# Performance work log

Hardware: AMD Instinct MI355X
Metric: run time of the kernel (lower is better)

## Reference

```python
import jax, jax.numpy as jnp
import numpy as np

B, S, D = 4, 2048, 2048
E = 64           # num_experts
TOPK = 2         # num_experts_per_token


def setup_inputs() -> dict:
    key = jax.random.key(0)
    k1, k2, k3 = jax.random.split(key, 3)
    x_real = jax.random.normal(k1, (B, S, D), dtype=jnp.float32)
    x_imag = jax.random.normal(k2, (B, S, D), dtype=jnp.float32)
    # flax Dense: kernel [in_features, out_features] with lecun_normal-ish scale
    W = jax.random.normal(k3, (2 * D, E), dtype=jnp.float32) / np.sqrt(2.0 * D)
    b = jnp.zeros((E,), dtype=jnp.float32)
    return {"x_real": x_real, "x_imag": x_imag, "W": W, "b": b}


def reference(x_real, x_imag, W, b):
    # amp = |x|, phase = angle(x) for x = x_real + i*x_imag
    amp = jnp.hypot(x_real, x_imag)                 # [B,S,D]
    phase = jnp.arctan2(x_imag, x_real)             # [B,S,D]
    routing_input = jnp.concatenate([amp, phase], axis=-1)  # [B,S,2D]
    scores = jnp.einsum('bsf,fe->bse', routing_input, W) + b  # [B,S,E]
    probs = jax.nn.softmax(scores, axis=-1)
    top_k_probs, top_k_indices = jax.lax.top_k(probs, TOPK)   # [B,S,K]
    top_k_probs = top_k_probs / jnp.sum(top_k_probs, axis=-1, keepdims=True)
    return (top_k_probs, top_k_indices)
```

## Files before the change

kernel.cpp:

```cpp
#include <hip/hip_runtime.h>
#include <math.h>

#define NTOK 8192
#define DD   2048
#define EE   64
#define TSTRIP 16
#define PROB_N (NTOK*2)
#define F_PSTRIDE (128*4*64*8)

typedef _Float16 f16x8 __attribute__((ext_vector_type(8)));
typedef _Float16 f16x4 __attribute__((ext_vector_type(4)));
typedef float    f32x4 __attribute__((ext_vector_type(4)));

__device__ __forceinline__ float fast_atan2f(float y, float x) {
    const float ax = __builtin_fabsf(x), ay = __builtin_fabsf(y);
    const float hi = fmaxf(ax, ay), lo = fminf(ax, ay);
    const bool  big = lo > 0.4142135679721832f * hi;
    const float num = big ? (lo - hi) : lo;
    const float den = big ? (lo + hi) : hi;
    float rc = __builtin_amdgcn_rcpf(den);
    rc = rc * fmaf(-den, rc, 2.0f);
    const float z  = num * rc;
    const float z2 = z * z;
    float p = fmaf(z2, 8.05374449538e-2f, -1.38776856032e-1f);
    p = fmaf(z2, p, 1.99777106478e-1f);
    p = fmaf(z2, p, -3.33329491539e-1f);
    float r = fmaf(z * z2, p, z);
    r = r + (big ? 0.78539816339744830962f : 0.0f);
    r = (ay > ax) ? (1.57079632679489661923f - r) : r;
    r = (x < 0.0f) ? (3.14159265358979323846f - r) : r;
    return copysignf(r, y);
}

__device__ __forceinline__ void fsplit2(float x, _Float16& h1, _Float16& h2s) {
    const _Float16 a = (_Float16)x;
    h1 = a;
    h2s = (_Float16)((x - (float)a) * 2048.0f);
}

__global__ __launch_bounds__(256) void wsplit(const float* __restrict__ W,
                                              _Float16* __restrict__ F) {
    const int g  = blockIdx.x * 256 + threadIdx.x;
    const int e  = g & 63;
    const int q  = g >> 6;
    const int d0 = q * 4;
    const int nt = e >> 4;
    const int lane = ((d0 & 31) >> 3) * 16 + (e & 15);
    const int j0 = d0 & 7;
    const int cka = 2 * (d0 >> 5);

    f16x4 a1, a2, p1, p2;
    #pragma unroll
    for (int i = 0; i < 4; ++i) {
        _Float16 h, l;
        fsplit2(W[(size_t)(d0 + i) * EE + e], h, l);      a1[i] = h; a2[i] = l;
        fsplit2(W[(size_t)(DD + d0 + i) * EE + e], h, l); p1[i] = h; p2[i] = l;
    }
    *(f16x4*)&F[((size_t)(0 * 128 + cka)     * 4 + nt) * 512 + lane * 8 + j0] = a1;
    *(f16x4*)&F[((size_t)(1 * 128 + cka)     * 4 + nt) * 512 + lane * 8 + j0] = a2;
    *(f16x4*)&F[((size_t)(0 * 128 + cka + 1) * 4 + nt) * 512 + lane * 8 + j0] = p1;
    *(f16x4*)&F[((size_t)(1 * 128 + cka + 1) * 4 + nt) * 512 + lane * 8 + j0] = p2;
}

__global__ __launch_bounds__(512) void gemm_topk(
    const float* __restrict__ xr, const float* __restrict__ xi,
    const _Float16* __restrict__ F, const float* __restrict__ bias,
    float* __restrict__ out)
{
    __shared__ float scoreP[8][TSTRIP][EE];

    const int tid = threadIdx.x;
    const int t0  = blockIdx.x * TSTRIP;
    const int wv = tid >> 6, lane = tid & 63;
    const int fm = lane & 15, fq = lane >> 4;

    const float* prx = xr + (size_t)(t0 + fm) * DD + wv * 256 + fq * 8;
    const float* pix = xi + (size_t)(t0 + fm) * DD + wv * 256 + fq * 8;

    f32x4 accH[4], accL[4];
    #pragma unroll
    for (int nt = 0; nt < 4; ++nt) {
        accH[nt] = (f32x4){0.f, 0.f, 0.f, 0.f};
        accL[nt] = (f32x4){0.f, 0.f, 0.f, 0.f};
    }

    #pragma unroll 2
    for (int p = 0; p < 8; ++p) {
        const float4 r0 = *(const float4*)(prx + p * 32);
        const float4 r1 = *(const float4*)(prx + p * 32 + 4);
        const float4 i0 = *(const float4*)(pix + p * 32);
        const float4 i1 = *(const float4*)(pix + p * 32 + 4);

        f16x8 a1, a2, q1, q2;
        #pragma unroll
        for (int h = 0; h < 2; ++h) {
            const float4 vr = h ? r1 : r0;
            const float4 vi = h ? i1 : i0;
            const float ar[4] = {vr.x, vr.y, vr.z, vr.w};
            const float ai[4] = {vi.x, vi.y, vi.z, vi.w};
            #pragma unroll
            for (int i = 0; i < 4; ++i) {
                const float amp = __builtin_amdgcn_sqrtf(fmaf(ar[i], ar[i], ai[i] * ai[i]));
                const float ph  = fast_atan2f(ai[i], ar[i]);
                _Float16 hh, ll;
                fsplit2(amp, hh, ll); a1[h * 4 + i] = hh; a2[h * 4 + i] = ll;
                fsplit2(ph,  hh, ll); q1[h * 4 + i] = hh; q2[h * 4 + i] = ll;
            }
        }

        const int ck = (wv * 8 + p) * 2;
        const _Float16* bp = F + ((size_t)ck * 4) * 512 + lane * 8;
        #pragma unroll
        for (int nt = 0; nt < 4; ++nt) {
            const _Float16* qp = bp + nt * 512;
            const f16x8 b1a = *(const f16x8*)(qp);
            const f16x8 b2a = *(const f16x8*)(qp + F_PSTRIDE);
            const f16x8 b1p = *(const f16x8*)(qp + 2048);
            const f16x8 b2p = *(const f16x8*)(qp + 2048 + F_PSTRIDE);
            accH[nt] = __builtin_amdgcn_mfma_f32_16x16x32_f16(a1, b1a, accH[nt], 0, 0, 0);
            accL[nt] = __builtin_amdgcn_mfma_f32_16x16x32_f16(a1, b2a, accL[nt], 0, 0, 0);
            accL[nt] = __builtin_amdgcn_mfma_f32_16x16x32_f16(a2, b1a, accL[nt], 0, 0, 0);
            accH[nt] = __builtin_amdgcn_mfma_f32_16x16x32_f16(q1, b1p, accH[nt], 0, 0, 0);
            accL[nt] = __builtin_amdgcn_mfma_f32_16x16x32_f16(q1, b2p, accL[nt], 0, 0, 0);
            accL[nt] = __builtin_amdgcn_mfma_f32_16x16x32_f16(q2, b1p, accL[nt], 0, 0, 0);
        }
    }

    #pragma unroll
    for (int nt = 0; nt < 4; ++nt)
        #pragma unroll
        for (int r = 0; r < 4; ++r)
            scoreP[wv][fq * 4 + r][nt * 16 + fm] =
                fmaf(accL[nt][r], 4.8828125e-4f, accH[nt][r]);
    __syncthreads();

    const float bv = bias[lane];
    #pragma unroll
    for (int rep = 0; rep < 2; ++rep) {
        const int tok = wv * 2 + rep;
        float v1 = bv;
        #pragma unroll
        for (int kq = 0; kq < 8; ++kq) v1 += scoreP[kq][tok][lane];
        float v2 = -INFINITY;
        int   i1 = lane, i2 = 64;
        #pragma unroll
        for (int off = 1; off < 64; off <<= 1) {
            const float ov1 = __shfl_xor(v1, off, 64);
            const int   oi1 = __shfl_xor(i1, off, 64);
            const float ov2 = __shfl_xor(v2, off, 64);
            const int   oi2 = __shfl_xor(i2, off, 64);
            const bool b1 = (ov1 > v1) || (ov1 == v1 && oi1 < i1);
            const float n1 = b1 ? ov1 : v1;  const int ni1 = b1 ? oi1 : i1;
            const float c1 = b1 ? v1  : ov1; const int ci1 = b1 ? i1  : oi1;
            const float c2 = b1 ? ov2 : v2;  const int ci2 = b1 ? oi2 : i2;
            const bool b2 = (c1 > c2) || (c1 == c2 && ci1 < ci2);
            v1 = n1; i1 = ni1;
            v2 = b2 ? c1 : c2; i2 = b2 ? ci1 : ci2;
        }
        if (lane == 0) {
            const int t = t0 + tok;
            const float z  = expf(v2 - v1);
            const float p1 = 1.0f / (1.0f + z);
            const float p2 = z / (1.0f + z);
            out[(size_t)t * 2 + 0] = p1;
            out[(size_t)t * 2 + 1] = p2;
            out[PROB_N + (size_t)t * 2 + 0] = (float)i1;
            out[PROB_N + (size_t)t * 2 + 1] = (float)i2;
        }
    }
}

extern "C" void kernel_launch(void* const* d_in, const int* in_sizes, int n_in,
                              void* d_out, int out_size, void* d_ws, size_t ws_size,
                              hipStream_t stream) {
    const float* xr = (const float*)d_in[0];
    const float* xi = (const float*)d_in[1];
    const float* W  = (const float*)d_in[2];
    const float* b  = (const float*)d_in[3];
    float* out = (float*)d_out;
    _Float16* F = (_Float16*)d_ws;

    wsplit<<<128, 256, 0, stream>>>(W, F);
    gemm_topk<<<NTOK / TSTRIP, 512, 0, stream>>>(xr, xi, F, b, out);
}
```

Measured before the change: 175.2 us.

## Software-pipeline x and weight loads with inline-asm global loads and vmcnt waits

```diff
diff --git a/kernel.cpp b/kernel.cpp
--- a/kernel.cpp
+++ b/kernel.cpp
@@ -11,6 +11,21 @@
 typedef _Float16 f16x8 __attribute__((ext_vector_type(8)));
 typedef _Float16 f16x4 __attribute__((ext_vector_type(4)));
 typedef float    f32x4 __attribute__((ext_vector_type(4)));
+
+__device__ __forceinline__ f16x8 gload_f16x8(const _Float16* p) {
+    f16x8 r;
+    asm volatile("global_load_dwordx4 %0, %1, off" : "=v"(r) : "v"(p));
+    return r;
+}
+__device__ __forceinline__ f32x4 gload_f32x4(const float* p) {
+    f32x4 r;
+    asm volatile("global_load_dwordx4 %0, %1, off" : "=v"(r) : "v"(p));
+    return r;
+}
+#define VMWAIT(n) do { \
+    asm volatile("s_waitcnt vmcnt(" #n ")" ::: "memory"); \
+    __builtin_amdgcn_sched_barrier(0); \
+} while (0)
 
 __device__ __forceinline__ float fast_atan2f(float y, float x) {
     const float ax = __builtin_fabsf(x), ay = __builtin_fabsf(y);
@@ -76,6 +91,7 @@
 
     const float* prx = xr + (size_t)(t0 + fm) * DD + wv * 256 + fq * 8;
     const float* pix = xi + (size_t)(t0 + fm) * DD + wv * 256 + fq * 8;
+    const _Float16* bp0 = F + (size_t)wv * 32768 + lane * 8;
 
     f32x4 accH[4], accL[4];
     #pragma unroll
@@ -84,39 +100,71 @@
         accL[nt] = (f32x4){0.f, 0.f, 0.f, 0.f};
     }
 
-    #pragma unroll 2
+    f32x4 xv[2][4];
+    f16x8 bb[2][16];
+
+    xv[0][0] = gload_f32x4(prx);
+    xv[0][1] = gload_f32x4(prx + 4);
+    xv[0][2] = gload_f32x4(pix);
+    xv[0][3] = gload_f32x4(pix + 4);
+    #pragma unroll
+    for (int nt = 0; nt < 4; ++nt) {
+        bb[0][nt * 4 + 0] = gload_f16x8(bp0 + nt * 512);
+        bb[0][nt * 4 + 1] = gload_f16x8(bp0 + nt * 512 + F_PSTRIDE);
+        bb[0][nt * 4 + 2] = gload_f16x8(bp0 + nt * 512 + 2048);
+        bb[0][nt * 4 + 3] = gload_f16x8(bp0 + nt * 512 + 2048 + F_PSTRIDE);
+    }
+    xv[1][0] = gload_f32x4(prx + 32);
+    xv[1][1] = gload_f32x4(prx + 36);
+    xv[1][2] = gload_f32x4(pix + 32);
+    xv[1][3] = gload_f32x4(pix + 36);
+
+    #pragma unroll 8
     for (int p = 0; p < 8; ++p) {
-        const float4 r0 = *(const float4*)(prx + p * 32);
-        const float4 r1 = *(const float4*)(prx + p * 32 + 4);
-        const float4 i0 = *(const float4*)(pix + p * 32);
-        const float4 i1 = *(const float4*)(pix + p * 32 + 4);
+        const int s = p & 1, ns = s ^ 1;
+
+        if (p < 7) { VMWAIT(20); } else { VMWAIT(16); }
 
         f16x8 a1, a2, q1, q2;
-        #pragma unroll
-        for (int h = 0; h < 2; ++h) {
-            const float4 vr = h ? r1 : r0;
-            const float4 vi = h ? i1 : i0;
-            const float ar[4] = {vr.x, vr.y, vr.z, vr.w};
-            const float ai[4] = {vi.x, vi.y, vi.z, vi.w};
+        {
+            const f32x4 vr0 = xv[s][0], vr1 = xv[s][1];
+            const f32x4 vi0 = xv[s][2], vi1 = xv[s][3];
             #pragma unroll
             for (int i = 0; i < 4; ++i) {
-                const float amp = __builtin_amdgcn_sqrtf(fmaf(ar[i], ar[i], ai[i] * ai[i]));
-                const float ph  = fast_atan2f(ai[i], ar[i]);
+                float rr = vr0[i], im = vi0[i];
+                float amp = __builtin_amdgcn_sqrtf(fmaf(rr, rr, im * im));
+                float ph  = fast_atan2f(im, rr);
                 _Float16 hh, ll;
-                fsplit2(amp, hh, ll); a1[h * 4 + i] = hh; a2[h * 4 + i] = ll;
-                fsplit2(ph,  hh, ll); q1[h * 4 + i] = hh; q2[h * 4 + i] = ll;
+                fsplit2(amp, hh, ll); a1[i] = hh; a2[i] = ll;
+                fsplit2(ph,  hh, ll); q1[i] = hh; q2[i] = ll;
+                rr = vr1[i]; im = vi1[i];
+                amp = __builtin_amdgcn_sqrtf(fmaf(rr, rr, im * im));
+                ph  = fast_atan2f(im, rr);
+                fsplit2(amp, hh, ll); a1[4 + i] = hh; a2[4 + i] = ll;
+                fsplit2(ph,  hh, ll); q1[4 + i] = hh; q2[4 + i] = ll;
             }
         }
 
-        const int ck = (wv * 8 + p) * 2;
-        const _Float16* bp = F + ((size_t)ck * 4) * 512 + lane * 8;
+        if (p < 7) {
+            const _Float16* nb = bp0 + (size_t)(p + 1) * 4096;
+            #pragma unroll
+            for (int nt = 0; nt < 4; ++nt) {
+                bb[ns][nt * 4 + 0] = gload_f16x8(nb + nt * 512);
+                bb[ns][nt * 4 + 1] = gload_f16x8(nb + nt * 512 + F_PSTRIDE);
+                bb[ns][nt * 4 + 2] = gload_f16x8(nb + nt * 512 + 2048);
+                bb[ns][nt * 4 + 3] = gload_f16x8(nb + nt * 512 + 2048 + F_PSTRIDE);
+            }
+            VMWAIT(20);
+        } else {
+            VMWAIT(0);
+        }
+
         #pragma unroll
         for (int nt = 0; nt < 4; ++nt) {
-            const _Float16* qp = bp + nt * 512;
-            const f16x8 b1a = *(const f16x8*)(qp);
-            const f16x8 b2a = *(const f16x8*)(qp + F_PSTRIDE);
-            const f16x8 b1p = *(const f16x8*)(qp + 2048);
-            const f16x8 b2p = *(const f16x8*)(qp + 2048 + F_PSTRIDE);
+            const f16x8 b1a = bb[s][nt * 4 + 0];
+            const f16x8 b2a = bb[s][nt * 4 + 1];
+            const f16x8 b1p = bb[s][nt * 4 + 2];
+            const f16x8 b2p = bb[s][nt * 4 + 3];
             accH[nt] = __builtin_amdgcn_mfma_f32_16x16x32_f16(a1, b1a, accH[nt], 0, 0, 0);
             accL[nt] = __builtin_amdgcn_mfma_f32_16x16x32_f16(a1, b2a, accL[nt], 0, 0, 0);
             accL[nt] = __builtin_amdgcn_mfma_f32_16x16x32_f16(a2, b1a, accL[nt], 0, 0, 0);
@@ -124,6 +172,13 @@
             accL[nt] = __builtin_amdgcn_mfma_f32_16x16x32_f16(q1, b2p, accL[nt], 0, 0, 0);
             accL[nt] = __builtin_amdgcn_mfma_f32_16x16x32_f16(q2, b1p, accL[nt], 0, 0, 0);
         }
+
+        if (p < 6) {
+            xv[s][0] = gload_f32x4(prx + (p + 2) * 32);
+            xv[s][1] = gload_f32x4(prx + (p + 2) * 32 + 4);
+            xv[s][2] = gload_f32x4(pix + (p + 2) * 32);
+            xv[s][3] = gload_f32x4(pix + (p + 2) * 32 + 4);
+        }
     }
 
     #pragma unroll
@@ -135,6 +190,7 @@
     __syncthreads();
 
     const float bv = bias[lane];
+
     #pragma unroll
     for (int rep = 0; rep < 2; ++rep) {
         const int tok = wv * 2 + rep;
```

Result: no change. 173.7 us (-0.9%).

## Process two 16-token strips per block to reuse weight fragments

Applied to the files above, without the earlier changes.

```diff
diff --git a/kernel.cpp b/kernel.cpp
--- a/kernel.cpp
+++ b/kernel.cpp
@@ -4,7 +4,7 @@
 #define NTOK 8192
 #define DD   2048
 #define EE   64
-#define TSTRIP 16
+#define TSTRIP 32
 #define PROB_N (NTOK*2)
 #define F_PSTRIDE (128*4*64*8)
 
@@ -67,31 +67,29 @@
     const _Float16* __restrict__ F, const float* __restrict__ bias,
     float* __restrict__ out)
 {
-    __shared__ float scoreP[8][TSTRIP][EE];
+    __shared__ float scoreP[8][TSTRIP][EE + 1];
 
     const int tid = threadIdx.x;
     const int t0  = blockIdx.x * TSTRIP;
     const int wv = tid >> 6, lane = tid & 63;
     const int fm = lane & 15, fq = lane >> 4;
 
-    const float* prx = xr + (size_t)(t0 + fm) * DD + wv * 256 + fq * 8;
-    const float* pix = xi + (size_t)(t0 + fm) * DD + wv * 256 + fq * 8;
-
-    f32x4 accH[4], accL[4];
+    const float* prx0 = xr + (size_t)(t0 + fm) * DD + wv * 256 + fq * 8;
+    const float* pix0 = xi + (size_t)(t0 + fm) * DD + wv * 256 + fq * 8;
+    const float* prx1 = prx0 + 16 * DD;
+    const float* pix1 = pix0 + 16 * DD;
+
+    f32x4 accH0[4], accL0[4], accH1[4], accL1[4];
     #pragma unroll
     for (int nt = 0; nt < 4; ++nt) {
-        accH[nt] = (f32x4){0.f, 0.f, 0.f, 0.f};
-        accL[nt] = (f32x4){0.f, 0.f, 0.f, 0.f};
-    }
-
-    #pragma unroll 2
-    for (int p = 0; p < 8; ++p) {
-        const float4 r0 = *(const float4*)(prx + p * 32);
-        const float4 r1 = *(const float4*)(prx + p * 32 + 4);
-        const float4 i0 = *(const float4*)(pix + p * 32);
-        const float4 i1 = *(const float4*)(pix + p * 32 + 4);
-
-        f16x8 a1, a2, q1, q2;
+        accH0[nt] = (f32x4){0.f, 0.f, 0.f, 0.f};
+        accL0[nt] = (f32x4){0.f, 0.f, 0.f, 0.f};
+        accH1[nt] = (f32x4){0.f, 0.f, 0.f, 0.f};
+        accL1[nt] = (f32x4){0.f, 0.f, 0.f, 0.f};
+    }
+
+    auto xform = [&](float4 r0, float4 r1, float4 i0, float4 i1,
+                     f16x8& a1, f16x8& a2, f16x8& q1, f16x8& q2) {
         #pragma unroll
         for (int h = 0; h < 2; ++h) {
             const float4 vr = h ? r1 : r0;
@@ -107,6 +105,22 @@
                 fsplit2(ph,  hh, ll); q1[h * 4 + i] = hh; q2[h * 4 + i] = ll;
             }
         }
+    };
+
+    #pragma unroll 2
+    for (int p = 0; p < 8; ++p) {
+        const float4 r00 = *(const float4*)(prx0 + p * 32);
+        const float4 r01 = *(const float4*)(prx0 + p * 32 + 4);
+        const float4 i00 = *(const float4*)(pix0 + p * 32);
+        const float4 i01 = *(const float4*)(pix0 + p * 32 + 4);
+        const float4 r10 = *(const float4*)(prx1 + p * 32);
+        const float4 r11 = *(const float4*)(prx1 + p * 32 + 4);
+        const float4 i10 = *(const float4*)(pix1 + p * 32);
+        const float4 i11 = *(const float4*)(pix1 + p * 32 + 4);
+
+        f16x8 a1_0, a2_0, q1_0, q2_0, a1_1, a2_1, q1_1, q2_1;
+        xform(r00, r01, i00, i01, a1_0, a2_0, q1_0, q2_0);
+        xform(r10, r11, i10, i11, a1_1, a2_1, q1_1, q2_1);
 
         const int ck = (wv * 8 + p) * 2;
         const _Float16* bp = F + ((size_t)ck * 4) * 512 + lane * 8;
@@ -117,27 +131,36 @@
             const f16x8 b2a = *(const f16x8*)(qp + F_PSTRIDE);
             const f16x8 b1p = *(const f16x8*)(qp + 2048);
             const f16x8 b2p = *(const f16x8*)(qp + 2048 + F_PSTRIDE);
-            accH[nt] = __builtin_amdgcn_mfma_f32_16x16x32_f16(a1, b1a, accH[nt], 0, 0, 0);
-            accL[nt] = __builtin_amdgcn_mfma_f32_16x16x32_f16(a1, b2a, accL[nt], 0, 0, 0);
-            accL[nt] = __builtin_amdgcn_mfma_f32_16x16x32_f16(a2, b1a, accL[nt], 0, 0, 0);
-            accH[nt] = __builtin_amdgcn_mfma_f32_16x16x32_f16(q1, b1p, accH[nt], 0, 0, 0);
-            accL[nt] = __builtin_amdgcn_mfma_f32_16x16x32_f16(q1, b2p, accL[nt], 0, 0, 0);
-            accL[nt] = __builtin_amdgcn_mfma_f32_16x16x32_f16(q2, b1p, accL[nt], 0, 0, 0);
+            accH0[nt] = __builtin_amdgcn_mfma_f32_16x16x32_f16(a1_0, b1a, accH0[nt], 0, 0, 0);
+            accL0[nt] = __builtin_amdgcn_mfma_f32_16x16x32_f16(a1_0, b2a, accL0[nt], 0, 0, 0);
+            accL0[nt] = __builtin_amdgcn_mfma_f32_16x16x32_f16(a2_0, b1a, accL0[nt], 0, 0, 0);
+            accH0[nt] = __builtin_amdgcn_mfma_f32_16x16x32_f16(q1_0, b1p, accH0[nt], 0, 0, 0);
+            accL0[nt] = __builtin_amdgcn_mfma_f32_16x16x32_f16(q1_0, b2p, accL0[nt], 0, 0, 0);
+            accL0[nt] = __builtin_amdgcn_mfma_f32_16x16x32_f16(q2_0, b1p, accL0[nt], 0, 0, 0);
+            accH1[nt] = __builtin_amdgcn_mfma_f32_16x16x32_f16(a1_1, b1a, accH1[nt], 0, 0, 0);
+            accL1[nt] = __builtin_amdgcn_mfma_f32_16x16x32_f16(a1_1, b2a, accL1[nt], 0, 0, 0);
+            accL1[nt] = __builtin_amdgcn_mfma_f32_16x16x32_f16(a2_1, b1a, accL1[nt], 0, 0, 0);
+            accH1[nt] = __builtin_amdgcn_mfma_f32_16x16x32_f16(q1_1, b1p, accH1[nt], 0, 0, 0);
+            accL1[nt] = __builtin_amdgcn_mfma_f32_16x16x32_f16(q1_1, b2p, accL1[nt], 0, 0, 0);
+            accL1[nt] = __builtin_amdgcn_mfma_f32_16x16x32_f16(q2_1, b1p, accL1[nt], 0, 0, 0);
         }
     }
 
     #pragma unroll
     for (int nt = 0; nt < 4; ++nt)
         #pragma unroll
-        for (int r = 0; r < 4; ++r)
+        for (int r = 0; r < 4; ++r) {
             scoreP[wv][fq * 4 + r][nt * 16 + fm] =
-                fmaf(accL[nt][r], 4.8828125e-4f, accH[nt][r]);
+                fmaf(accL0[nt][r], 4.8828125e-4f, accH0[nt][r]);
+            scoreP[wv][16 + fq * 4 + r][nt * 16 + fm] =
+                fmaf(accL1[nt][r], 4.8828125e-4f, accH1[nt][r]);
+        }
     __syncthreads();
 
     const float bv = bias[lane];
     #pragma unroll
-    for (int rep = 0; rep < 2; ++rep) {
-        const int tok = wv * 2 + rep;
+    for (int rep = 0; rep < 4; ++rep) {
+        const int tok = wv * 4 + rep;
         float v1 = bv;
         #pragma unroll
         for (int kq = 0; kq < 8; ++kq) v1 += scoreP[kq][tok][lane];
```

New measurement: 170.3 us. -2.8%, faster.

## Stage x tiles through padded LDS with coalesced row loads

Applied to the files above, without the earlier changes.

```diff
diff --git a/kernel.cpp b/kernel.cpp
--- a/kernel.cpp
+++ b/kernel.cpp
@@ -7,6 +7,7 @@
 #define TSTRIP 16
 #define PROB_N (NTOK*2)
 #define F_PSTRIDE (128*4*64*8)
+#define XROW 516
 
 typedef _Float16 f16x8 __attribute__((ext_vector_type(8)));
 typedef _Float16 f16x4 __attribute__((ext_vector_type(4)));
@@ -67,15 +68,19 @@
     const _Float16* __restrict__ F, const float* __restrict__ bias,
     float* __restrict__ out)
 {
-    __shared__ float scoreP[8][TSTRIP][EE];
+    __shared__ __align__(16) float SBUF[2 * 16 * XROW];
+    float* XR = SBUF;
+    float* XI = SBUF + 16 * XROW;
+    float* scoreP = SBUF;
 
     const int tid = threadIdx.x;
     const int t0  = blockIdx.x * TSTRIP;
     const int wv = tid >> 6, lane = tid & 63;
     const int fm = lane & 15, fq = lane >> 4;
 
-    const float* prx = xr + (size_t)(t0 + fm) * DD + wv * 256 + fq * 8;
-    const float* pix = xi + (size_t)(t0 + fm) * DD + wv * 256 + fq * 8;
+    const int soff = tid * 4;
+    const int srow = soff >> 9;
+    const int scol = soff & 511;
 
     f32x4 accH[4], accL[4];
     #pragma unroll
@@ -84,53 +89,69 @@
         accL[nt] = (f32x4){0.f, 0.f, 0.f, 0.f};
     }
 
-    #pragma unroll 2
-    for (int p = 0; p < 8; ++p) {
-        const float4 r0 = *(const float4*)(prx + p * 32);
-        const float4 r1 = *(const float4*)(prx + p * 32 + 4);
-        const float4 i0 = *(const float4*)(pix + p * 32);
-        const float4 i1 = *(const float4*)(pix + p * 32 + 4);
-
-        f16x8 a1, a2, q1, q2;
-        #pragma unroll
-        for (int h = 0; h < 2; ++h) {
-            const float4 vr = h ? r1 : r0;
-            const float4 vi = h ? i1 : i0;
-            const float ar[4] = {vr.x, vr.y, vr.z, vr.w};
-            const float ai[4] = {vi.x, vi.y, vi.z, vi.w};
+    for (int s = 0; s < 4; ++s) {
+        const float* gxr = xr + (size_t)t0 * DD + s * 512;
+        const float* gxi = xi + (size_t)t0 * DD + s * 512;
+        #pragma unroll
+        for (int k = 0; k < 4; ++k) {
+            const int row = srow + k * 4;
+            const float4 vr = *(const float4*)(gxr + (size_t)row * DD + scol);
+            const float4 vi = *(const float4*)(gxi + (size_t)row * DD + scol);
+            *(float4*)&XR[row * XROW + scol] = vr;
+            *(float4*)&XI[row * XROW + scol] = vi;
+        }
+        __syncthreads();
+
+        #pragma unroll
+        for (int j = 0; j < 2; ++j) {
+            const int cb = (2 * wv + j) * 32 + fq * 8;
+            const float4 r0 = *(const float4*)&XR[fm * XROW + cb];
+            const float4 r1 = *(const float4*)&XR[fm * XROW + cb + 4];
+            const float4 i0 = *(const float4*)&XI[fm * XROW + cb];
+            const float4 i1 = *(const float4*)&XI[fm * XROW + cb + 4];
+
+            f16x8 a1, a2, q1, q2;
             #pragma unroll
-            for (int i = 0; i < 4; ++i) {
-                const float amp = __builtin_amdgcn_sqrtf(fmaf(ar[i], ar[i], ai[i] * ai[i]));
-                const float ph  = fast_atan2f(ai[i], ar[i]);
-                _Float16 hh, ll;
-                fsplit2(amp, hh, ll); a1[h * 4 + i] = hh; a2[h * 4 + i] = ll;
-                fsplit2(ph,  hh, ll); q1[h * 4 + i] = hh; q2[h * 4 + i] = ll;
+            for (int h = 0; h < 2; ++h) {
+                const float4 vr = h ? r1 : r0;
+                const float4 vi = h ? i1 : i0;
+                const float ar[4] = {vr.x, vr.y, vr.z, vr.w};
+                const float ai[4] = {vi.x, vi.y, vi.z, vi.w};
+                #pragma unroll
+                for (int i = 0; i < 4; ++i) {
+                    const float amp = __builtin_amdgcn_sqrtf(fmaf(ar[i], ar[i], ai[i] * ai[i]));
+                    const float ph  = fast_atan2f(ai[i], ar[i]);
+                    _Float16 hh, ll;
+                    fsplit2(amp, hh, ll); a1[h * 4 + i] = hh; a2[h * 4 + i] = ll;
+                    fsplit2(ph,  hh, ll); q1[h * 4 + i] = hh; q2[h * 4 + i] = ll;
+                }
             }
-        }
-
-        const int ck = (wv * 8 + p) * 2;
-        const _Float16* bp = F + ((size_t)ck * 4) * 512 + lane * 8;
-        #pragma unroll
-        for (int nt = 0; nt < 4; ++nt) {
-            const _Float16* qp = bp + nt * 512;
-            const f16x8 b1a = *(const f16x8*)(qp);
-            const f16x8 b2a = *(const f16x8*)(qp + F_PSTRIDE);
-            const f16x8 b1p = *(const f16x8*)(qp + 2048);
-            const f16x8 b2p = *(const f16x8*)(qp + 2048 + F_PSTRIDE);
-            accH[nt] = __builtin_amdgcn_mfma_f32_16x16x32_f16(a1, b1a, accH[nt], 0, 0, 0);
-            accL[nt] = __builtin_amdgcn_mfma_f32_16x16x32_f16(a1, b2a, accL[nt], 0, 0, 0);
-            accL[nt] = __builtin_amdgcn_mfma_f32_16x16x32_f16(a2, b1a, accL[nt], 0, 0, 0);
-            accH[nt] = __builtin_amdgcn_mfma_f32_16x16x32_f16(q1, b1p, accH[nt], 0, 0, 0);
-            accL[nt] = __builtin_amdgcn_mfma_f32_16x16x32_f16(q1, b2p, accL[nt], 0, 0, 0);
-            accL[nt] = __builtin_amdgcn_mfma_f32_16x16x32_f16(q2, b1p, accL[nt], 0, 0, 0);
-        }
+
+            const int g = s * 16 + 2 * wv + j;
+            const _Float16* bp = F + ((size_t)(2 * g) * 4) * 512 + lane * 8;
+            #pragma unroll
+            for (int nt = 0; nt < 4; ++nt) {
+                const _Float16* qp = bp + nt * 512;
+                const f16x8 b1a = *(const f16x8*)(qp);
+                const f16x8 b2a = *(const f16x8*)(qp + F_PSTRIDE);
+                const f16x8 b1p = *(const f16x8*)(qp + 2048);
+                const f16x8 b2p = *(const f16x8*)(qp + 2048 + F_PSTRIDE);
+                accH[nt] = __builtin_amdgcn_mfma_f32_16x16x32_f16(a1, b1a, accH[nt], 0, 0, 0);
+                accL[nt] = __builtin_amdgcn_mfma_f32_16x16x32_f16(a1, b2a, accL[nt], 0, 0, 0);
+                accL[nt] = __builtin_amdgcn_mfma_f32_16x16x32_f16(a2, b1a, accL[nt], 0, 0, 0);
+                accH[nt] = __builtin_amdgcn_mfma_f32_16x16x32_f16(q1, b1p, accH[nt], 0, 0, 0);
+                accL[nt] = __builtin_amdgcn_mfma_f32_16x16x32_f16(q1, b2p, accL[nt], 0, 0, 0);
+                accL[nt] = __builtin_amdgcn_mfma_f32_16x16x32_f16(q2, b1p, accL[nt], 0, 0, 0);
+            }
+        }
+        __syncthreads();
     }
 
     #pragma unroll
     for (int nt = 0; nt < 4; ++nt)
         #pragma unroll
         for (int r = 0; r < 4; ++r)
-            scoreP[wv][fq * 4 + r][nt * 16 + fm] =
+            scoreP[((wv * 16) + fq * 4 + r) * 64 + nt * 16 + fm] =
                 fmaf(accL[nt][r], 4.8828125e-4f, accH[nt][r]);
     __syncthreads();
 
@@ -140,7 +161,7 @@
         const int tok = wv * 2 + rep;
         float v1 = bv;
         #pragma unroll
-        for (int kq = 0; kq < 8; ++kq) v1 += scoreP[kq][tok][lane];
+        for (int kq = 0; kq < 8; ++kq) v1 += scoreP[(kq * 16 + tok) * 64 + lane];
         float v2 = -INFINITY;
         int   i1 = lane, i2 = 64;
         #pragma unroll
```

New measurement: 170.2 us. 1.03x faster.
